# Kernel tuning notes

Hardware: AMD Instinct MI355X
Metric: run time of the kernel (lower is better)

Reference implementation:

```python
import jax, jax.numpy as jnp
import numpy as np
from jax import lax

B = 256; D_IN = 2048; HID = 2048; NSEG = 10; D_CTX = 1024; OUT = 100; NI = 205
KW_PCT = 0.05
K = int(round(KW_PCT * HID))  # 102 winners per sample per layer
W_DENSITY = 0.05      # weight_sparsity = 0.95
DEND_DENSITY = 0.05   # dendrite_weight_sparsity = 0.95


def setup_inputs() -> dict:
    key = jax.random.key(0)
    ks = jax.random.split(key, 16)
    def u(k, shape, bound):
        return jax.random.uniform(k, shape, minval=-bound, maxval=bound, dtype=jnp.float32)
    inp = {}
    inp["x"] = jax.random.normal(ks[0], (B, D_IN), jnp.float32)
    inp["context"] = jax.random.normal(ks[1], (B, D_CTX), jnp.float32)
    # layer 1 FF weights: modified kaiming, input density 1.0 -> bound = 1/sqrt(fan_in)
    inp["W1"] = u(ks[2], (HID, D_IN), 1.0 / np.sqrt(D_IN))
    inp["b1"] = jnp.zeros((HID,), jnp.float32)
    # dendrites: input density 1.0 (context_percent_on=1), weight density 0.05
    dend_bound = 1.0 / np.sqrt(DEND_DENSITY * D_CTX)
    inp["segW1"] = u(ks[3], (HID, NSEG, D_CTX), dend_bound)
    inp["maskW1"] = (jax.random.uniform(ks[4], (HID, D_IN)) < W_DENSITY).astype(jnp.float32)
    inp["maskS1"] = (jax.random.uniform(ks[5], (HID, NSEG, D_CTX)) < DEND_DENSITY).astype(jnp.float32)
    # layer 2 FF weights: input density = kw_percent_on (k-winners upstream)
    inp["W2"] = u(ks[6], (HID, HID), 1.0 / np.sqrt(KW_PCT * HID))
    inp["b2"] = jnp.zeros((HID,), jnp.float32)
    inp["segW2"] = u(ks[7], (HID, NSEG, D_CTX), dend_bound)
    inp["maskW2"] = (jax.random.uniform(ks[8], (HID, HID)) < W_DENSITY).astype(jnp.float32)
    inp["maskS2"] = (jax.random.uniform(ks[9], (HID, NSEG, D_CTX)) < DEND_DENSITY).astype(jnp.float32)
    # Dale (EiDense) output head: non-negative excitatory/inhibitory factors
    s = 1.0 / np.sqrt(HID)
    inp["Wex_out"] = jax.random.uniform(ks[10], (OUT, HID), dtype=jnp.float32) * s
    inp["Wix_out"] = jax.random.uniform(ks[11], (1, HID), dtype=jnp.float32) * s
    inp["Wei_out"] = jax.random.uniform(ks[12], (OUT, 1), dtype=jnp.float32)
    inp["b_out"] = jnp.zeros((OUT,), jnp.float32)
    return inp


def _kwinners(y, k):
    # keep top-k activations per row, zero the rest (boost_strength=0)
    vals, idxs = lax.top_k(y, k)  # [B, k]
    rows = jnp.arange(y.shape[0])[:, None]
    return jnp.zeros_like(y).at[rows, idxs].set(vals)


def _dendritic_layer(x, context, W, b, segW, maskW, maskS):
    # sparse-masked feedforward projection
    y = x @ (W * maskW).T + b  # [B, HID]
    # per-unit dendrite segment activations from context
    d = jnp.einsum('bc,usc->bus', context, segW * maskS)  # [B, HID, NSEG]
    # absolute-max gating: pick segment with max |activation|, gate by sigmoid
    sel = jnp.argmax(jnp.abs(d), axis=-1)  # [B, HID]
    chosen = jnp.take_along_axis(d, sel[..., None], axis=-1)[..., 0]
    y = y * jax.nn.sigmoid(chosen)
    return _kwinners(y, K)


def reference(x, context, W1, b1, segW1, maskW1, maskS1, W2, b2, segW2, maskW2, maskS2, Wex_out, Wix_out, Wei_out, b_out):
    h = _dendritic_layer(x, context, W1, b1, segW1, maskW1, maskS1)
    h = _dendritic_layer(h, context, W2, b2, segW2, maskW2, maskS2)
    # EiDense output head: W = Wex - Wei @ Wix (Dale's law), no output nonlinearity
    W_out = Wex_out - Wei_out @ Wix_out  # [OUT, HID]
    return h @ W_out.T + b_out
```

## Files before the change

kernel.cpp:

```cpp
#include <hip/hip_runtime.h>
#include <math.h>

#define B_SZ   256
#define D_IN   2048
#define HID    2048
#define NSEG   10
#define D_CTX  1024
#define OUT_N  100
#define KWIN   102
#define CAP    256

__device__ __forceinline__ unsigned f2key(float f) {
  unsigned b = __float_as_uint(f);
  return (b & 0x80000000u) ? ~b : (b | 0x80000000u);
}
__device__ __forceinline__ float key2f(unsigned k) {
  return (k & 0x80000000u) ? __uint_as_float(k & 0x7FFFFFFFu) : __uint_as_float(~k);
}

__global__ __launch_bounds__(256) void transpose_k(const float* __restrict__ src,
                                                   float* __restrict__ dst,
                                                   int rows, int cols) {
  __shared__ float tile[32][33];
  int c0 = blockIdx.x * 32, r0 = blockIdx.y * 32;
  int tx = threadIdx.x, ty = threadIdx.y;
  for (int i = ty; i < 32; i += 8)
    tile[i][tx] = src[(r0 + i) * cols + (c0 + tx)];
  __syncthreads();
  for (int i = ty; i < 32; i += 8)
    dst[(c0 + i) * rows + (r0 + tx)] = tile[tx][i];
}

__device__ __forceinline__ int compact_seg(const float* __restrict__ wrow,
                                           const float* __restrict__ mrow,
                                           int len4, float2* pairs, int* scnt) {
  const int t = threadIdx.x;
  if (t == 0) *scnt = 0;
  __syncthreads();
  const float4* __restrict__ w4 = (const float4*)wrow;
  const float4* __restrict__ m4 = (const float4*)mrow;
  for (int e = t; e < len4; e += 64) {
    float4 w = w4[e];
    float4 m = m4[e];
    bool n0 = (m.x != 0.f), n1 = (m.y != 0.f), n2 = (m.z != 0.f), n3 = (m.w != 0.f);
    int nz = (int)n0 + (int)n1 + (int)n2 + (int)n3;
    if (nz) {
      int pos = atomicAdd(scnt, nz);
      int c = e << 2;
      if (n0) { if (pos < CAP) pairs[pos] = make_float2(w.x, __int_as_float(c));     pos++; }
      if (n1) { if (pos < CAP) pairs[pos] = make_float2(w.y, __int_as_float(c + 1)); pos++; }
      if (n2) { if (pos < CAP) pairs[pos] = make_float2(w.z, __int_as_float(c + 2)); pos++; }
      if (n3) { if (pos < CAP) pairs[pos] = make_float2(w.w, __int_as_float(c + 3)); pos++; }
    }
  }
  __syncthreads();
  int c = *scnt;
  return c > CAP ? CAP : c;
}

__device__ __forceinline__ void gather_dot(const float* __restrict__ src,
                                           const float2* pairs, int cnt,
                                           int t4, float out4[4]) {
  float acc[4][4];
#pragma unroll
  for (int s = 0; s < 4; ++s)
#pragma unroll
    for (int i = 0; i < 4; ++i) acc[s][i] = 0.f;
  int j = 0;
  for (; j + 4 <= cnt; j += 4) {
#pragma unroll
    for (int s = 0; s < 4; ++s) {
      float2 p = pairs[j + s];
      const float4 cv = *(const float4*)(src + (__float_as_int(p.y) << 8) + t4);
      acc[s][0] += cv.x * p.x; acc[s][1] += cv.y * p.x;
      acc[s][2] += cv.z * p.x; acc[s][3] += cv.w * p.x;
    }
  }
  for (; j < cnt; ++j) {
    float2 p = pairs[j];
    const float4 cv = *(const float4*)(src + (__float_as_int(p.y) << 8) + t4);
    acc[0][0] += cv.x * p.x; acc[0][1] += cv.y * p.x;
    acc[0][2] += cv.z * p.x; acc[0][3] += cv.w * p.x;
  }
#pragma unroll
  for (int i = 0; i < 4; ++i)
    out4[i] = (acc[0][i] + acc[1][i]) + (acc[2][i] + acc[3][i]);
}

__global__ __launch_bounds__(64) void dend_kernel(
    const float* __restrict__ W1, const float* __restrict__ maskW1, const float* __restrict__ b1,
    const float* __restrict__ segW1, const float* __restrict__ maskS1,
    const float* __restrict__ segW2, const float* __restrict__ maskS2,
    const float* __restrict__ xT, const float* __restrict__ ctxT,
    float* __restrict__ y1T, float* __restrict__ gate2T) {
  __shared__ float2 pairs[CAP];
  __shared__ int scnt;
  const int t = threadIdx.x, t4 = t * 4;
  const int bid = blockIdx.x;
  float bestA[4] = {-1.f, -1.f, -1.f, -1.f};
  float chosen[4] = {0.f, 0.f, 0.f, 0.f};

  if (bid < HID) {
    const int u = bid;
    int cnt = compact_seg(W1 + u * D_IN, maskW1 + u * D_IN, D_IN / 4, pairs, &scnt);
    float ff[4];
    gather_dot(xT, pairs, cnt, t4, ff);
    for (int s = 0; s < NSEG; ++s) {
      const int r = (u * NSEG + s) * D_CTX;
      cnt = compact_seg(segW1 + r, maskS1 + r, D_CTX / 4, pairs, &scnt);
      float d[4];
      gather_dot(ctxT, pairs, cnt, t4, d);
#pragma unroll
      for (int i = 0; i < 4; ++i) {
        float a = fabsf(d[i]);
        if (a > bestA[i]) { bestA[i] = a; chosen[i] = d[i]; }
      }
    }
    float bb = b1[u];
    float4 o;
    o.x = (ff[0] + bb) / (1.f + expf(-chosen[0]));
    o.y = (ff[1] + bb) / (1.f + expf(-chosen[1]));
    o.z = (ff[2] + bb) / (1.f + expf(-chosen[2]));
    o.w = (ff[3] + bb) / (1.f + expf(-chosen[3]));
    *(float4*)(y1T + u * B_SZ + t4) = o;
  } else {
    const int u = bid - HID;
    for (int s = 0; s < NSEG; ++s) {
      const int r = (u * NSEG + s) * D_CTX;
      int cnt = compact_seg(segW2 + r, maskS2 + r, D_CTX / 4, pairs, &scnt);
      float d[4];
      gather_dot(ctxT, pairs, cnt, t4, d);
#pragma unroll
      for (int i = 0; i < 4; ++i) {
        float a = fabsf(d[i]);
        if (a > bestA[i]) { bestA[i] = a; chosen[i] = d[i]; }
      }
    }
    float4 g;
    g.x = 1.f / (1.f + expf(-chosen[0]));
    g.y = 1.f / (1.f + expf(-chosen[1]));
    g.z = 1.f / (1.f + expf(-chosen[2]));
    g.w = 1.f / (1.f + expf(-chosen[3]));
    *(float4*)(gate2T + u * B_SZ + t4) = g;
  }
}

__global__ __launch_bounds__(64) void ff2_kernel(
    const float* __restrict__ W2, const float* __restrict__ maskW2, const float* __restrict__ b2,
    const float* __restrict__ h1T, const float* __restrict__ gate2T, float* __restrict__ y2T) {
  __shared__ float2 pairs[CAP];
  __shared__ int scnt;
  const int t = threadIdx.x, t4 = t * 4, u = blockIdx.x;
  int cnt = compact_seg(W2 + u * HID, maskW2 + u * HID, HID / 4, pairs, &scnt);
  float acc[4];
  gather_dot(h1T, pairs, cnt, t4, acc);
  float bb = b2[u];
  float4 g = *(const float4*)(gate2T + u * B_SZ + t4);
  float4 o;
  o.x = (acc[0] + bb) * g.x; o.y = (acc[1] + bb) * g.y;
  o.z = (acc[2] + bb) * g.z; o.w = (acc[3] + bb) * g.w;
  *(float4*)(y2T + u * B_SZ + t4) = o;
}

__global__ __launch_bounds__(256) void topk_kernel(const float* __restrict__ yT,
                                                   float* __restrict__ dst, int mode) {
  const int b = blockIdx.x, t = threadIdx.x;
  __shared__ int hist[256];
  __shared__ int sfx[256];
  __shared__ unsigned sPref;
  __shared__ int sRem;
  unsigned myk[8];
#pragma unroll
  for (int i = 0; i < 8; ++i) {
    int u = t * 8 + i;
    myk[i] = f2key(yT[u * B_SZ + b]);
  }
  unsigned pref = 0;
  int rem = KWIN;
  for (int shift = 24; shift >= 0; shift -= 8) {
    hist[t] = 0;
    __syncthreads();
    unsigned hiMask = (shift == 24) ? 0u : (0xFFFFFFFFu << (shift + 8));
#pragma unroll
    for (int i = 0; i < 8; ++i) {
      unsigned k = myk[i];
      if ((k & hiMask) == pref) atomicAdd(&hist[(k >> shift) & 255], 1);
    }
    __syncthreads();
    sfx[t] = hist[t];
    __syncthreads();
    for (int off = 1; off < 256; off <<= 1) {
      int add = (t + off < 256) ? sfx[t + off] : 0;
      __syncthreads();
      sfx[t] += add;
      __syncthreads();
    }
    int s_incl = sfx[t];
    int s_excl = (t == 255) ? 0 : sfx[t + 1];
    if (s_incl >= rem && s_excl < rem) {
      sPref = pref | (((unsigned)t) << shift);
      sRem = rem - s_excl;
    }
    __syncthreads();
    pref = sPref;
    rem = sRem;
    __syncthreads();
  }
  int eq = 0;
#pragma unroll
  for (int i = 0; i < 8; ++i) eq += (myk[i] == pref) ? 1 : 0;
  sfx[t] = eq;
  __syncthreads();
  for (int off = 1; off < 256; off <<= 1) {
    int add = (t >= off) ? sfx[t - off] : 0;
    __syncthreads();
    sfx[t] += add;
    __syncthreads();
  }
  int excl = sfx[t] - eq;
  int taken = 0;
#pragma unroll
  for (int i = 0; i < 8; ++i) {
    unsigned k = myk[i];
    bool keep;
    if (k > pref) keep = true;
    else if (k == pref) { keep = (excl + taken) < rem; taken++; }
    else keep = false;
    float f = keep ? key2f(k) : 0.f;
    int u = t * 8 + i;
    if (mode == 0) dst[u * B_SZ + b] = f;
    else dst[b * HID + u] = f;
  }
}

__global__ __launch_bounds__(256) void out_kernel(
    const float* __restrict__ h2, const float* __restrict__ Wex, const float* __restrict__ Wix,
    const float* __restrict__ Wei, const float* __restrict__ bo, float* __restrict__ out) {
  const int b = blockIdx.x, t = threadIdx.x;
  __shared__ float hrow[HID];
  __shared__ float red[256];
  float part = 0.f;
#pragma unroll
  for (int i = 0; i < 8; ++i) {
    int u = t + 256 * i;
    float v = h2[b * HID + u];
    hrow[u] = v;
    part += v * Wix[u];
  }
  red[t] = part;
  __syncthreads();
  for (int off = 128; off > 0; off >>= 1) {
    if (t < off) red[t] += red[t + off];
    __syncthreads();
  }
  float S = red[0];
  const int w = t >> 6, l = t & 63;
  for (int o = w; o < OUT_N; o += 4) {
    float acc = 0.f;
    const float* wr = Wex + o * HID;
#pragma unroll
    for (int q = 0; q < HID / 64; ++q) acc += hrow[l + 64 * q] * wr[l + 64 * q];
    for (int off = 32; off > 0; off >>= 1) acc += __shfl_down(acc, off, 64);
    if (l == 0) out[b * OUT_N + o] = acc - Wei[o] * S + bo[o];
  }
}

extern "C" void kernel_launch(void* const* d_in, const int* in_sizes, int n_in,
                              void* d_out, int out_size, void* d_ws, size_t ws_size,
                              hipStream_t stream) {
  const float* x      = (const float*)d_in[0];
  const float* ctx    = (const float*)d_in[1];
  const float* W1     = (const float*)d_in[2];
  const float* b1     = (const float*)d_in[3];
  const float* segW1  = (const float*)d_in[4];
  const float* maskW1 = (const float*)d_in[5];
  const float* maskS1 = (const float*)d_in[6];
  const float* W2     = (const float*)d_in[7];
  const float* b2     = (const float*)d_in[8];
  const float* segW2  = (const float*)d_in[9];
  const float* maskW2 = (const float*)d_in[10];
  const float* maskS2 = (const float*)d_in[11];
  const float* Wex    = (const float*)d_in[12];
  const float* Wix    = (const float*)d_in[13];
  const float* Wei    = (const float*)d_in[14];
  const float* bo     = (const float*)d_in[15];
  float* out = (float*)d_out;
  float* ws = (float*)d_ws;

  float* xT     = ws;
  float* ctxT   = ws + 524288;
  float* y1T    = ws + 786432;
  float* gate2T = ws + 1310720;
  float* h1T    = ws + 1835008;
  float* y2T    = ws + 2359296;
  float* h2     = ws + 2883584;

  dim3 tb(32, 8);
  transpose_k<<<dim3(D_IN / 32, B_SZ / 32), tb, 0, stream>>>(x, xT, B_SZ, D_IN);
  transpose_k<<<dim3(D_CTX / 32, B_SZ / 32), tb, 0, stream>>>(ctx, ctxT, B_SZ, D_CTX);
  dend_kernel<<<2 * HID, 64, 0, stream>>>(W1, maskW1, b1, segW1, maskS1, segW2, maskS2,
                                          xT, ctxT, y1T, gate2T);
  topk_kernel<<<B_SZ, 256, 0, stream>>>(y1T, h1T, 0);
  ff2_kernel<<<HID, 64, 0, stream>>>(W2, maskW2, b2, h1T, gate2T, y2T);
  topk_kernel<<<B_SZ, 256, 0, stream>>>(y2T, h2, 1);
  out_kernel<<<B_SZ, 256, 0, stream>>>(h2, Wex, Wix, Wei, bo, out);
}
```

Measured before the change: 588.1 us.

## Pack four rows per block, nontemporal weight loads, coalesced top-k via transposes

Dendrite and FF2 kernels now run four independent 64-thread waves per 256-thread block, each with its own shared pair buffer. Weight and mask streams use nontemporal loads, and gather_dot unrolls eight pairs per step. Top-k now reads and writes rows in place with vector loads, and explicit transpose kernels are added before and after it. This replaces the strided column access in top-k at the cost of extra launches and extra memory passes.

After: 519.9 us. 1.13x faster.

```diff
diff --git a/kernel.cpp b/kernel.cpp
--- a/kernel.cpp
+++ b/kernel.cpp
@@ -10,6 +10,12 @@
 #define KWIN   102
 #define CAP    256
 
+typedef float f32x4 __attribute__((ext_vector_type(4)));
+
+__device__ __forceinline__ f32x4 ntld4(const float* p) {
+  return __builtin_nontemporal_load((const f32x4*)p);
+}
+
 __device__ __forceinline__ unsigned f2key(float f) {
   unsigned b = __float_as_uint(f);
   return (b & 0x80000000u) ? ~b : (b | 0x80000000u);
@@ -34,14 +40,12 @@
 __device__ __forceinline__ int compact_seg(const float* __restrict__ wrow,
                                            const float* __restrict__ mrow,
                                            int len4, float2* pairs, int* scnt) {
-  const int t = threadIdx.x;
+  const int t = threadIdx.x & 63;
   if (t == 0) *scnt = 0;
   __syncthreads();
-  const float4* __restrict__ w4 = (const float4*)wrow;
-  const float4* __restrict__ m4 = (const float4*)mrow;
   for (int e = t; e < len4; e += 64) {
-    float4 w = w4[e];
-    float4 m = m4[e];
+    f32x4 w = ntld4(wrow + 4 * e);
+    f32x4 m = ntld4(mrow + 4 * e);
     bool n0 = (m.x != 0.f), n1 = (m.y != 0.f), n2 = (m.z != 0.f), n3 = (m.w != 0.f);
     int nz = (int)n0 + (int)n1 + (int)n2 + (int)n3;
     if (nz) {
@@ -67,18 +71,18 @@
 #pragma unroll
     for (int i = 0; i < 4; ++i) acc[s][i] = 0.f;
   int j = 0;
-  for (; j + 4 <= cnt; j += 4) {
-#pragma unroll
-    for (int s = 0; s < 4; ++s) {
+  for (; j + 8 <= cnt; j += 8) {
+#pragma unroll
+    for (int s = 0; s < 8; ++s) {
       float2 p = pairs[j + s];
-      const float4 cv = *(const float4*)(src + (__float_as_int(p.y) << 8) + t4);
-      acc[s][0] += cv.x * p.x; acc[s][1] += cv.y * p.x;
-      acc[s][2] += cv.z * p.x; acc[s][3] += cv.w * p.x;
+      const f32x4 cv = *(const f32x4*)(src + (__float_as_int(p.y) << 8) + t4);
+      acc[s & 3][0] += cv.x * p.x; acc[s & 3][1] += cv.y * p.x;
+      acc[s & 3][2] += cv.z * p.x; acc[s & 3][3] += cv.w * p.x;
     }
   }
   for (; j < cnt; ++j) {
     float2 p = pairs[j];
-    const float4 cv = *(const float4*)(src + (__float_as_int(p.y) << 8) + t4);
+    const f32x4 cv = *(const f32x4*)(src + (__float_as_int(p.y) << 8) + t4);
     acc[0][0] += cv.x * p.x; acc[0][1] += cv.y * p.x;
     acc[0][2] += cv.z * p.x; acc[0][3] += cv.w * p.x;
   }
@@ -87,27 +91,31 @@
     out4[i] = (acc[0][i] + acc[1][i]) + (acc[2][i] + acc[3][i]);
 }
 
-__global__ __launch_bounds__(64) void dend_kernel(
+__global__ __launch_bounds__(256, 4) void dend_kernel(
     const float* __restrict__ W1, const float* __restrict__ maskW1, const float* __restrict__ b1,
     const float* __restrict__ segW1, const float* __restrict__ maskS1,
     const float* __restrict__ segW2, const float* __restrict__ maskS2,
     const float* __restrict__ xT, const float* __restrict__ ctxT,
     float* __restrict__ y1T, float* __restrict__ gate2T) {
-  __shared__ float2 pairs[CAP];
-  __shared__ int scnt;
-  const int t = threadIdx.x, t4 = t * 4;
-  const int bid = blockIdx.x;
+  __shared__ float2 pairs_s[4][CAP];
+  __shared__ int scnt_s[4];
+  const int wave = threadIdx.x >> 6;
+  const int t = threadIdx.x & 63, t4 = t * 4;
+  float2* pairs = pairs_s[wave];
+  int* scnt = &scnt_s[wave];
+  const int row = blockIdx.x * 4 + wave;
+
   float bestA[4] = {-1.f, -1.f, -1.f, -1.f};
   float chosen[4] = {0.f, 0.f, 0.f, 0.f};
 
-  if (bid < HID) {
-    const int u = bid;
-    int cnt = compact_seg(W1 + u * D_IN, maskW1 + u * D_IN, D_IN / 4, pairs, &scnt);
+  if (row < HID) {
+    const int u = row;
+    int cnt = compact_seg(W1 + u * D_IN, maskW1 + u * D_IN, D_IN / 4, pairs, scnt);
     float ff[4];
     gather_dot(xT, pairs, cnt, t4, ff);
     for (int s = 0; s < NSEG; ++s) {
       const int r = (u * NSEG + s) * D_CTX;
-      cnt = compact_seg(segW1 + r, maskS1 + r, D_CTX / 4, pairs, &scnt);
+      cnt = compact_seg(segW1 + r, maskS1 + r, D_CTX / 4, pairs, scnt);
       float d[4];
       gather_dot(ctxT, pairs, cnt, t4, d);
 #pragma unroll
@@ -124,10 +132,10 @@
     o.w = (ff[3] + bb) / (1.f + expf(-chosen[3]));
     *(float4*)(y1T + u * B_SZ + t4) = o;
   } else {
-    const int u = bid - HID;
+    const int u = row - HID;
     for (int s = 0; s < NSEG; ++s) {
       const int r = (u * NSEG + s) * D_CTX;
-      int cnt = compact_seg(segW2 + r, maskS2 + r, D_CTX / 4, pairs, &scnt);
+      int cnt = compact_seg(segW2 + r, maskS2 + r, D_CTX / 4, pairs, scnt);
       float d[4];
       gather_dot(ctxT, pairs, cnt, t4, d);
 #pragma unroll
@@ -145,15 +153,17 @@
   }
 }
 
-__global__ __launch_bounds__(64) void ff2_kernel(
+__global__ __launch_bounds__(256, 4) void ff2_kernel(
     const float* __restrict__ W2, const float* __restrict__ maskW2, const float* __restrict__ b2,
     const float* __restrict__ h1T, const float* __restrict__ gate2T, float* __restrict__ y2T) {
-  __shared__ float2 pairs[CAP];
-  __shared__ int scnt;
-  const int t = threadIdx.x, t4 = t * 4, u = blockIdx.x;
-  int cnt = compact_seg(W2 + u * HID, maskW2 + u * HID, HID / 4, pairs, &scnt);
+  __shared__ float2 pairs_s[4][CAP];
+  __shared__ int scnt_s[4];
+  const int wave = threadIdx.x >> 6;
+  const int t = threadIdx.x & 63, t4 = t * 4;
+  const int u = blockIdx.x * 4 + wave;
+  int cnt = compact_seg(W2 + u * HID, maskW2 + u * HID, HID / 4, pairs_s[wave], &scnt_s[wave]);
   float acc[4];
-  gather_dot(h1T, pairs, cnt, t4, acc);
+  gather_dot(h1T, pairs_s[wave], cnt, t4, acc);
   float bb = b2[u];
   float4 g = *(const float4*)(gate2T + u * B_SZ + t4);
   float4 o;
@@ -162,19 +172,18 @@
   *(float4*)(y2T + u * B_SZ + t4) = o;
 }
 
-__global__ __launch_bounds__(256) void topk_kernel(const float* __restrict__ yT,
-                                                   float* __restrict__ dst, int mode) {
+__global__ __launch_bounds__(256) void topk_kernel(float* __restrict__ y) {
   const int b = blockIdx.x, t = threadIdx.x;
   __shared__ int hist[256];
   __shared__ int sfx[256];
   __shared__ unsigned sPref;
   __shared__ int sRem;
+  float* __restrict__ row = y + b * HID;
   unsigned myk[8];
-#pragma unroll
-  for (int i = 0; i < 8; ++i) {
-    int u = t * 8 + i;
-    myk[i] = f2key(yT[u * B_SZ + b]);
-  }
+  f32x4 v0 = *(const f32x4*)(row + t * 8);
+  f32x4 v1 = *(const f32x4*)(row + t * 8 + 4);
+  myk[0] = f2key(v0.x); myk[1] = f2key(v0.y); myk[2] = f2key(v0.z); myk[3] = f2key(v0.w);
+  myk[4] = f2key(v1.x); myk[5] = f2key(v1.y); myk[6] = f2key(v1.z); myk[7] = f2key(v1.w);
   unsigned pref = 0;
   int rem = KWIN;
   for (int shift = 24; shift >= 0; shift -= 8) {
@@ -219,6 +228,7 @@
   }
   int excl = sfx[t] - eq;
   int taken = 0;
+  float o[8];
 #pragma unroll
   for (int i = 0; i < 8; ++i) {
     unsigned k = myk[i];
@@ -226,11 +236,12 @@
     if (k > pref) keep = true;
     else if (k == pref) { keep = (excl + taken) < rem; taken++; }
     else keep = false;
-    float f = keep ? key2f(k) : 0.f;
-    int u = t * 8 + i;
-    if (mode == 0) dst[u * B_SZ + b] = f;
-    else dst[b * HID + u] = f;
-  }
+    o[i] = keep ? key2f(k) : 0.f;
+  }
+  f32x4 w0 = {o[0], o[1], o[2], o[3]};
+  f32x4 w1 = {o[4], o[5], o[6], o[7]};
+  *(f32x4*)(row + t * 8) = w0;
+  *(f32x4*)(row + t * 8 + 4) = w1;
 }
 
 __global__ __launch_bounds__(256) void out_kernel(
@@ -290,18 +301,20 @@
   float* xT     = ws;
   float* ctxT   = ws + 524288;
   float* y1T    = ws + 786432;
-  float* gate2T = ws + 1310720;
+  float* bufA   = ws + 1310720;
   float* h1T    = ws + 1835008;
-  float* y2T    = ws + 2359296;
-  float* h2     = ws + 2883584;
+  float* gate2T = ws + 2359296;
 
   dim3 tb(32, 8);
   transpose_k<<<dim3(D_IN / 32, B_SZ / 32), tb, 0, stream>>>(x, xT, B_SZ, D_IN);
   transpose_k<<<dim3(D_CTX / 32, B_SZ / 32), tb, 0, stream>>>(ctx, ctxT, B_SZ, D_CTX);
-  dend_kernel<<<2 * HID, 64, 0, stream>>>(W1, maskW1, b1, segW1, maskS1, segW2, maskS2,
-                                          xT, ctxT, y1T, gate2T);
-  topk_kernel<<<B_SZ, 256, 0, stream>>>(y1T, h1T, 0);
-  ff2_kernel<<<HID, 64, 0, stream>>>(W2, maskW2, b2, h1T, gate2T, y2T);
-  topk_kernel<<<B_SZ, 256, 0, stream>>>(y2T, h2, 1);
-  out_kernel<<<B_SZ, 256, 0, stream>>>(h2, Wex, Wix, Wei, bo, out);
-}
+  dend_kernel<<<2 * HID / 4, 256, 0, stream>>>(W1, maskW1, b1, segW1, maskS1, segW2, maskS2,
+                                               xT, ctxT, y1T, gate2T);
+  transpose_k<<<dim3(B_SZ / 32, HID / 32), tb, 0, stream>>>(y1T, bufA, HID, B_SZ);
+  topk_kernel<<<B_SZ, 256, 0, stream>>>(bufA);
+  transpose_k<<<dim3(HID / 32, B_SZ / 32), tb, 0, stream>>>(bufA, h1T, B_SZ, HID);
+  ff2_kernel<<<HID / 4, 256, 0, stream>>>(W2, maskW2, b2, h1T, gate2T, y1T);
+  transpose_k<<<dim3(B_SZ / 32, HID / 32), tb, 0, stream>>>(y1T, bufA, HID, B_SZ);
+  topk_kernel<<<B_SZ, 256, 0, stream>>>(bufA);
+  out_kernel<<<B_SZ, 256, 0, stream>>>(bufA, Wex, Wix, Wei, bo, out);
+}
```
